# Performance work log

Hardware: AMD Instinct MI355X
Metric: run time of the kernel (lower is better)

The kernel has to match this reference:

```python
import jax, jax.numpy as jnp
from jax import lax
import numpy as np

PERCENTAGES = [0.004, 0.006, 0.008, 0.01, 0.012]
RADIUS = 1.0  # shape == 'square'
B, N = 4, 8192


def setup_inputs() -> dict:
    key = jax.random.key(0)
    adv_pcs = jax.random.uniform(key, (B, N, 3), dtype=jnp.float32)
    return {"adv_pcs": adv_pcs}


def _gather_points(pcs, idx):
    # pcs [B,N,3], idx [B,S] -> [B,S,3]
    idx3 = jnp.broadcast_to(idx[:, :, None], idx.shape + (3,))
    return jnp.take_along_axis(pcs, idx3, axis=1)


def farthest_point_sample(pcs, n_samples):
    # iterative FPS starting at index 0; returns indices [B, n_samples]
    Bb, Nn, _ = pcs.shape

    def step(carry, _):
        min_d2, last = carry  # [B,N], [B]
        p = _gather_points(pcs, last[:, None])  # [B,1,3]
        d2 = jnp.sum((pcs - p) ** 2, axis=-1)  # [B,N]
        min_d2 = jnp.minimum(min_d2, d2)
        nxt = jnp.argmax(min_d2, axis=-1).astype(jnp.int32)
        return (min_d2, nxt), last

    init = (jnp.full((Bb, Nn), 1e10, pcs.dtype), jnp.zeros((Bb,), jnp.int32))
    _, idx = lax.scan(step, init, None, length=n_samples)
    return jnp.transpose(idx)  # [B, n_samples]


def ball_query(seeds, pcs, r, K):
    # seeds [B,S,3], pcs [B,N,3] -> pts [B,S,K,3], idx [B,S,K] (-1 padded)
    d2 = jnp.sum((seeds[:, :, None, :] - pcs[:, None, :, :]) ** 2, axis=-1)  # [B,S,N]
    valid = d2 < r * r
    # stable sort: in-radius points first, preserving index order
    order = jnp.argsort(jnp.where(valid, 0, 1).astype(jnp.int32), axis=-1, stable=True)
    idx = order[..., :K]  # [B,S,K]
    cnt = jnp.sum(valid, axis=-1)  # [B,S]
    keep = jnp.arange(K)[None, None, :] < cnt[:, :, None]
    idx = jnp.where(keep, idx, -1)
    pts = jax.vmap(lambda p, i: p[i])(pcs, jnp.clip(idx, 0))  # [B,S,K,3]
    return pts, idx


def knn_second_sqdist(groups, lengths):
    # groups [G,K,3]; first `lengths[g]` rows of each group are valid candidates.
    # Returns squared distance to the 2nd nearest neighbor (incl. self at 0) [G,K].
    G, K, _ = groups.shape
    d2 = jnp.sum((groups[:, :, None, :] - groups[:, None, :, :]) ** 2, axis=-1)  # [G,K,K]
    col_ok = jnp.arange(K)[None, None, :] < lengths[:, None, None]
    d2 = jnp.where(col_ok, d2, jnp.inf)
    top2 = -lax.top_k(-d2, 2)[0]  # two smallest along candidates
    nn2 = top2[:, :, 1]  # second smallest (first is self, dist 0)
    return jnp.where(jnp.isfinite(nn2), nn2, 0.0)  # pad like pytorch3d (0 for missing)


def reference(adv_pcs):
    Bb, Nn, _ = adv_pcs.shape
    dt = adv_pcs.dtype
    seed_num = int(Nn * 0.05)
    fps_idx = farthest_point_sample(adv_pcs, seed_num)
    seeds = _gather_points(adv_pcs, fps_idx)  # [B,seed,3]
    loss = jnp.zeros((Bb,), dt)
    for p in PERCENTAGES:
        exp_num = Nn * p
        r = float(np.sqrt(p) * RADIUS)
        expect_dis = jnp.sqrt(jnp.asarray(np.pi * RADIUS ** 2 / exp_num * p, dt))
        K = int(2 * exp_num)
        pts, idx = ball_query(seeds, adv_pcs, r, K)
        pts = pts.reshape(Bb * seed_num, K, 3)
        idx = idx.reshape(Bb * seed_num, K)
        mask = idx != -1  # [G,K]
        gnum = jnp.sum(mask, axis=-1)  # [G], >= 1 (seed itself in-radius)
        nn2 = knn_second_sqdist(pts, gnum)  # [G,K] squared dists
        safe = jnp.where(nn2 > 0, nn2, 1.0)
        nn_dis = jnp.where(nn2 > 0, jnp.sqrt(safe), 0.0)
        clutter = jnp.square(nn_dis - expect_dis) / (expect_dis + 1e-12)
        # faithful to torch: sum over ALL elements, then elementwise divide by counts
        clutter_vec = jnp.sum(clutter * mask) / gnum.astype(dt)  # [G]
        imbalance = jnp.square(gnum.astype(dt) - exp_num) / exp_num  # [G]
        ul = (clutter_vec * imbalance).reshape(Bb, seed_num).mean(axis=-1)  # [B]
        loss = loss + ul
    return loss / len(PERCENTAGES)
```

## Files before the change

### kernel.cpp

```cpp
#include <hip/hip_runtime.h>
#include <math.h>

#define N_PTS 8192
#define B_SZ 4
#define SEED_NUM 409
#define FPS_THREADS 256
#define LTOT 653

typedef float f2 __attribute__((ext_vector_type(2)));
typedef float f4 __attribute__((ext_vector_type(4)));

__device__ __forceinline__ float sqdist(float ax, float ay, float az,
                                        float bx, float by, float bz) {
  float dx = __fsub_rn(ax, bx);
  float dy = __fsub_rn(ay, by);
  float dz = __fsub_rn(az, bz);
  return __fadd_rn(__fadd_rn(__fmul_rn(dx, dx), __fmul_rn(dy, dy)),
                   __fmul_rn(dz, dz));
}

#define FOR16(M) \
  M(0) M(1) M(2) M(3) M(4) M(5) M(6) M(7) \
  M(8) M(9) M(10) M(11) M(12) M(13) M(14) M(15)

template <int CTRL>
__device__ __forceinline__ unsigned long long dpp_u64_bc1(
    unsigned long long k) {
  const unsigned lo2 = (unsigned)__builtin_amdgcn_update_dpp(
      0, (int)(unsigned)k, CTRL, 0xf, 0xf, true);
  const unsigned hi2 = (unsigned)__builtin_amdgcn_update_dpp(
      0, (int)(unsigned)(k >> 32), CTRL, 0xf, 0xf, true);
  return ((unsigned long long)hi2 << 32) | lo2;
}
template <int CTRL, int ROW_MASK>
__device__ __forceinline__ unsigned long long dpp_u64_keep(
    unsigned long long k) {
  const unsigned lo2 = (unsigned)__builtin_amdgcn_update_dpp(
      (int)(unsigned)k, (int)(unsigned)k, CTRL, ROW_MASK, 0xf, false);
  const unsigned hi2 = (unsigned)__builtin_amdgcn_update_dpp(
      (int)(unsigned)(k >> 32), (int)(unsigned)(k >> 32), CTRL, ROW_MASK, 0xf,
      false);
  return ((unsigned long long)hi2 << 32) | lo2;
}

__global__ __launch_bounds__(FPS_THREADS, 1) void fps_kernel(
    const float* __restrict__ pcs, float* __restrict__ seeds,
    double* __restrict__ sums ) {
#pragma clang fp contract(off)
  const int b = blockIdx.x;
  const int tid = threadIdx.x;
  const int lane = tid & 63, wid = tid >> 6;
  const float* base = pcs + (size_t)b * N_PTS * 3;

  if (b == 0 && tid < 25) sums[tid] = 0.0;

  __shared__ f4 spts4[N_PTS];
  __shared__ float seedbuf[SEED_NUM * 3];
  __shared__ unsigned long long red[2][4];

#define FPS_DECL(j) f2 px##j, py##j, pz##j, md##j;
  FOR16(FPS_DECL)
#undef FPS_DECL

#define FPS_INIT(j)                                   \
  {                                                   \
    const int i0 = tid + (2 * (j)) * FPS_THREADS;     \
    const int i1 = i0 + FPS_THREADS;                  \
    px##j = (f2){base[i0 * 3 + 0], base[i1 * 3 + 0]}; \
    py##j = (f2){base[i0 * 3 + 1], base[i1 * 3 + 1]}; \
    pz##j = (f2){base[i0 * 3 + 2], base[i1 * 3 + 2]}; \
    md##j = (f2){1e10f, 1e10f};   \
    spts4[i0] = (f4){px##j.x, py##j.x, pz##j.x, 0.f}; \
    spts4[i1] = (f4){px##j.y, py##j.y, pz##j.y, 0.f}; \
  }
  FOR16(FPS_INIT)
#undef FPS_INIT

#define FPS_PIN(j) asm volatile("" : "+v"(px##j), "+v"(py##j), "+v"(pz##j));
  FOR16(FPS_PIN)
#undef FPS_PIN

  float cx = base[0], cy = base[1], cz = base[2];

  for (int s = 0; s < SEED_NUM; ++s) {
    if (tid == 0) {
      seedbuf[s * 3 + 0] = cx;
      seedbuf[s * 3 + 1] = cy;
      seedbuf[s * 3 + 2] = cz;
    }
    const f2 ccx = (f2){cx, cx}, ccy = (f2){cy, cy}, ccz = (f2){cz, cz};
    float bv = -1.0f;
    int bi = 0;
#define FPS_UPD(j)                                                      \
  {                                                                     \
    const f2 dx = px##j - ccx;                                          \
    const f2 dy = py##j - ccy;                                          \
    const f2 dz = pz##j - ccz;                                          \
    const f2 t0 = dx * dx;                                              \
    const f2 t1 = dy * dy;                                              \
    const f2 t2 = dz * dz;                                              \
    const f2 d2 = (t0 + t1) + t2;                                       \
    const f2 m = __builtin_elementwise_min(md##j, d2);                  \
    md##j = m;                                                          \
    if (m.x > bv) { bv = m.x; bi = tid + (2 * (j)) * FPS_THREADS; }     \
    if (m.y > bv) { bv = m.y; bi = tid + (2 * (j) + 1) * FPS_THREADS; } \
  }
    FOR16(FPS_UPD)
#undef FPS_UPD
    unsigned long long key =
        ((unsigned long long)__float_as_uint(bv) << 32) |
        (unsigned long long)(unsigned)(N_PTS - 1 - bi);
    unsigned long long o;
    o = dpp_u64_bc1<0x111>(key);         key = (o > key) ? o : key;
    o = dpp_u64_bc1<0x112>(key);         key = (o > key) ? o : key;
    o = dpp_u64_bc1<0x114>(key);         key = (o > key) ? o : key;
    o = dpp_u64_bc1<0x118>(key);         key = (o > key) ? o : key;
    o = dpp_u64_keep<0x142, 0xa>(key);   key = (o > key) ? o : key;
    o = dpp_u64_keep<0x143, 0xc>(key);   key = (o > key) ? o : key;
    if (lane == 63) red[s & 1][wid] = key;
    __syncthreads();
    unsigned long long kmax = red[s & 1][0];
#pragma unroll
    for (int w = 1; w < 4; ++w) {
      const unsigned long long t = red[s & 1][w];
      kmax = (t > kmax) ? t : kmax;
    }
    const int ci = N_PTS - 1 - (int)(unsigned)(kmax & 0xffffffffull);
    const f4 c = spts4[ci];
    cx = c.x;
    cy = c.y;
    cz = c.z;
  }

  __syncthreads();
  float* sg = seeds + (size_t)b * SEED_NUM * 3;
  for (int i = tid; i < SEED_NUM * 3; i += FPS_THREADS) sg[i] = seedbuf[i];
}

__global__ __launch_bounds__(256) void group_kernel(
    const float* __restrict__ pcs, const float* __restrict__ seeds,
    double* __restrict__ totS , double* __restrict__ accA ) {
  const int g = blockIdx.x;
  const int b = g / SEED_NUM;
  const int tid = threadIdx.x;
  const int lane = tid & 63, wid = tid >> 6;

  const int Kc[5] = {65, 98, 131, 163, 196};
  const int off[5] = {0, 65, 163, 294, 457};
  const double Pd[5] = {0.004, 0.006, 0.008, 0.01, 0.012};
  float r2c[5], expnf[5], expdc[5];
#pragma unroll
  for (int p = 0; p < 5; ++p) {
    const double pd = Pd[p];
    const double rd = sqrt(pd);
    r2c[p] = (float)(rd * rd);
    const double expn_d = 8192.0 * pd;
    expnf[p] = (float)expn_d;
    expdc[p] = sqrtf((float)(M_PI / expn_d * pd));
  }

  const float* base = pcs + (size_t)b * N_PTS * 3;
  const float* sp = seeds + (size_t)g * 3;
  const float sx = sp[0], sy = sp[1], sz = sp[2];

  __shared__ float lx[LTOT], ly[LTOT], lz[LTOT];
  __shared__ int cnt[5];
  __shared__ int wtot[4];
  __shared__ double wsum[4];

  if (tid < 5) cnt[tid] = 0;
  __syncthreads();

  const float r2max = r2c[4];
  for (int i = tid; i < N_PTS; i += 256) {
    const float x = base[i * 3 + 0];
    const float y = base[i * 3 + 1];
    const float z = base[i * 3 + 2];
    const float d2 = sqdist(x, y, z, sx, sy, sz);
    if (d2 < r2max) {
#pragma unroll
      for (int p = 0; p < 5; ++p) {
        if (d2 < r2c[p]) {
          const int pos = atomicAdd(&cnt[p], 1);
          if (pos < Kc[p]) {
            lx[off[p] + pos] = x;
            ly[off[p] + pos] = y;
            lz[off[p] + pos] = z;
          }
        }
      }
    }
  }
  __syncthreads();

#pragma unroll
  for (int p = 0; p < 5; ++p) {
    if (cnt[p] > Kc[p]) {
      int run = 0;
      for (int base_i = 0; base_i < N_PTS; base_i += 256) {
        const int i = base_i + tid;
        const float x = base[i * 3 + 0];
        const float y = base[i * 3 + 1];
        const float z = base[i * 3 + 2];
        const float d2 = sqdist(x, y, z, sx, sy, sz);
        const bool valid = d2 < r2c[p];
        const unsigned long long m = __ballot(valid);
        if (lane == 0) wtot[wid] = __popcll(m);
        __syncthreads();
        int pos = run + __popcll(m & ((1ull << lane) - 1ull));
        for (int w = 0; w < wid; ++w) pos += wtot[w];
        if (valid && pos < Kc[p]) {
          lx[off[p] + pos] = x; ly[off[p] + pos] = y; lz[off[p] + pos] = z;
        }
        run += wtot[0] + wtot[1] + wtot[2] + wtot[3];
        __syncthreads();
      }
    }
  }

#pragma unroll
  for (int p = 0; p < 5; ++p) {
    const int gn = min(cnt[p], Kc[p]);
    const float ed = expdc[p];
    const int lb = off[p];
    double localS = 0.0;
    for (int r0 = 0; r0 < gn; r0 += 64) {
      const int row = r0 + (tid >> 2);
      const int sub = tid & 3;
      float m1 = INFINITY, m2 = INFINITY;
      if (row < gn) {
        const float xi = lx[lb + row], yi = ly[lb + row], zi = lz[lb + row];
        for (int j = sub; j < gn; j += 4) {
          const float d2 = sqdist(xi, yi, zi, lx[lb + j], ly[lb + j], lz[lb + j]);
          if (d2 < m1) { m2 = m1; m1 = d2; }
          else if (d2 < m2) { m2 = d2; }
        }
      }
#pragma unroll
      for (int d = 1; d <= 2; d <<= 1) {
        const float om1 = __shfl_xor(m1, d);
        const float om2 = __shfl_xor(m2, d);
        const float lo = fminf(m1, om1);
        const float hi = fmaxf(m1, om1);
        m2 = fminf(fminf(m2, om2), hi);
        m1 = lo;
      }
      if (row < gn && sub == 0) {
        const float nn2 = (m2 > 1e37f) ? 0.0f : m2;
        const float nnd = (nn2 > 0.0f) ? sqrtf(nn2) : 0.0f;
        const float diff = __fsub_rn(nnd, ed);
        const float clut = __fdiv_rn(__fmul_rn(diff, diff),
                                     __fadd_rn(ed, 1e-12f));
        localS += (double)clut;
      }
    }
#pragma unroll
    for (int o = 32; o > 0; o >>= 1) localS += __shfl_down(localS, o);
    if (lane == 0) wsum[wid] = localS;
    __syncthreads();
    if (tid == 0) {
      const double S = wsum[0] + wsum[1] + wsum[2] + wsum[3];
      atomicAdd(&totS[p], S);
      const float gf = (float)gn;
      const float dd = __fsub_rn(gf, expnf[p]);
      const float imb = __fdiv_rn(__fmul_rn(dd, dd), expnf[p]);
      atomicAdd(&accA[p * 4 + b], (double)imb / (double)gf);
    }
    __syncthreads();
  }
}

__global__ void finalize_kernel(const double* __restrict__ totS,
                                const double* __restrict__ accA,
                                float* __restrict__ out) {
  const int b = threadIdx.x;
  if (b < B_SZ) {
    double acc = 0.0;
    for (int p = 0; p < 5; ++p)
      acc += totS[p] * (accA[p * 4 + b] / (double)SEED_NUM);
    out[b] = (float)(acc / 5.0);
  }
}

extern "C" void kernel_launch(void* const* d_in, const int* in_sizes, int n_in,
                              void* d_out, int out_size, void* d_ws,
                              size_t ws_size, hipStream_t stream) {
  (void)in_sizes; (void)n_in; (void)out_size; (void)ws_size;
  const float* pcs = (const float*)d_in[0];
  float* out = (float*)d_out;

  float* seeds = (float*)d_ws;
  double* sums = (double*)((char*)d_ws + 19632);

  fps_kernel<<<B_SZ, FPS_THREADS, 0, stream>>>(pcs, seeds, sums);
  group_kernel<<<B_SZ * SEED_NUM, 256, 0, stream>>>(pcs, seeds, sums, sums + 5);
  finalize_kernel<<<1, 64, 0, stream>>>(sums, sums + 5, out);
}
```

Baseline: 481.2 us.

## Fuse finalize into group kernel, pack points as float4, batch atomics

Removes the separate finalize launch: the last group block, detected through a global atomic counter, reads the accumulated sums and writes the output. Shared point storage moves from three SoA float arrays to a float4 array, so each neighbor is read with one vector LDS load. The per-percentage syncs and atomics are deferred to a single batched phase. The FPS reduction reads the four wave keys as two 128-bit loads. This adds a threadfence and counter atomic per block, and more shared memory for the float4 layout.

```diff
diff --git a/kernel.cpp b/kernel.cpp
--- a/kernel.cpp
+++ b/kernel.cpp
@@ -6,6 +6,7 @@
 #define SEED_NUM 409
 #define FPS_THREADS 256
 #define LTOT 653
+#define N_GROUPS (B_SZ * SEED_NUM)
 
 typedef float f2 __attribute__((ext_vector_type(2)));
 typedef float f4 __attribute__((ext_vector_type(4)));
@@ -52,11 +53,11 @@
   const int lane = tid & 63, wid = tid >> 6;
   const float* base = pcs + (size_t)b * N_PTS * 3;
 
-  if (b == 0 && tid < 25) sums[tid] = 0.0;
+  if (b == 0 && tid < 26) sums[tid] = 0.0;
 
   __shared__ f4 spts4[N_PTS];
   __shared__ float seedbuf[SEED_NUM * 3];
-  __shared__ unsigned long long red[2][4];
+  __shared__ __align__(16) unsigned long long red[2][4];
 
 #define FPS_DECL(j) f2 px##j, py##j, pz##j, md##j;
   FOR16(FPS_DECL)
@@ -119,12 +120,12 @@
     o = dpp_u64_keep<0x143, 0xc>(key);   key = (o > key) ? o : key;
     if (lane == 63) red[s & 1][wid] = key;
     __syncthreads();
-    unsigned long long kmax = red[s & 1][0];
-#pragma unroll
-    for (int w = 1; w < 4; ++w) {
-      const unsigned long long t = red[s & 1][w];
-      kmax = (t > kmax) ? t : kmax;
-    }
+    const ulonglong2* rp = (const ulonglong2*)(&red[s & 1][0]);
+    const ulonglong2 r01 = rp[0];
+    const ulonglong2 r23 = rp[1];
+    const unsigned long long ka = (r01.y > r01.x) ? r01.y : r01.x;
+    const unsigned long long kb = (r23.y > r23.x) ? r23.y : r23.x;
+    const unsigned long long kmax = (kb > ka) ? kb : ka;
     const int ci = N_PTS - 1 - (int)(unsigned)(kmax & 0xffffffffull);
     const f4 c = spts4[ci];
     cx = c.x;
@@ -139,7 +140,8 @@
 
 __global__ __launch_bounds__(256) void group_kernel(
     const float* __restrict__ pcs, const float* __restrict__ seeds,
-    double* __restrict__ totS , double* __restrict__ accA ) {
+    double* __restrict__ totS , double* __restrict__ accA ,
+    unsigned int* __restrict__ dcnt, float* __restrict__ out) {
   const int g = blockIdx.x;
   const int b = g / SEED_NUM;
   const int tid = threadIdx.x;
@@ -163,10 +165,11 @@
   const float* sp = seeds + (size_t)g * 3;
   const float sx = sp[0], sy = sp[1], sz = sp[2];
 
-  __shared__ float lx[LTOT], ly[LTOT], lz[LTOT];
+  __shared__ f4 lpt[LTOT];
   __shared__ int cnt[5];
   __shared__ int wtot[4];
-  __shared__ double wsum[4];
+  __shared__ double wsum[5][4];
+  __shared__ int islast;
 
   if (tid < 5) cnt[tid] = 0;
   __syncthreads();
@@ -183,9 +186,7 @@
         if (d2 < r2c[p]) {
           const int pos = atomicAdd(&cnt[p], 1);
           if (pos < Kc[p]) {
-            lx[off[p] + pos] = x;
-            ly[off[p] + pos] = y;
-            lz[off[p] + pos] = z;
+            lpt[off[p] + pos] = (f4){x, y, z, 0.f};
           }
         }
       }
@@ -210,7 +211,7 @@
         int pos = run + __popcll(m & ((1ull << lane) - 1ull));
         for (int w = 0; w < wid; ++w) pos += wtot[w];
         if (valid && pos < Kc[p]) {
-          lx[off[p] + pos] = x; ly[off[p] + pos] = y; lz[off[p] + pos] = z;
+          lpt[off[p] + pos] = (f4){x, y, z, 0.f};
         }
         run += wtot[0] + wtot[1] + wtot[2] + wtot[3];
         __syncthreads();
@@ -229,9 +230,10 @@
       const int sub = tid & 3;
       float m1 = INFINITY, m2 = INFINITY;
       if (row < gn) {
-        const float xi = lx[lb + row], yi = ly[lb + row], zi = lz[lb + row];
+        const f4 pi = lpt[lb + row];
         for (int j = sub; j < gn; j += 4) {
-          const float d2 = sqdist(xi, yi, zi, lx[lb + j], ly[lb + j], lz[lb + j]);
+          const f4 pj = lpt[lb + j];
+          const float d2 = sqdist(pi.x, pi.y, pi.z, pj.x, pj.y, pj.z);
           if (d2 < m1) { m2 = m1; m1 = d2; }
           else if (d2 < m2) { m2 = d2; }
         }
@@ -256,29 +258,43 @@
     }
 #pragma unroll
     for (int o = 32; o > 0; o >>= 1) localS += __shfl_down(localS, o);
-    if (lane == 0) wsum[wid] = localS;
+    if (lane == 0) wsum[p][wid] = localS;
+  }
+  __syncthreads();
+
+  if (tid < 5) {
+    const double S = wsum[tid][0] + wsum[tid][1] + wsum[tid][2] + wsum[tid][3];
+    atomicAdd(&totS[tid], S);
+  } else if (tid < 10) {
+    const int p = tid - 5;
+    const int gn = min(cnt[p], Kc[p]);
+    const float gf = (float)gn;
+    const float dd = __fsub_rn(gf, expnf[p]);
+    const float imb = __fdiv_rn(__fmul_rn(dd, dd), expnf[p]);
+    atomicAdd(&accA[p * 4 + b], (double)imb / (double)gf);
+  }
+
+  __syncthreads();
+  if (tid == 0) {
+    __threadfence();
+    const unsigned int old = atomicAdd(dcnt, 1u);
+    islast = (old == (unsigned int)(N_GROUPS - 1)) ? 1 : 0;
+  }
+  __syncthreads();
+  if (islast) {
+    __shared__ double fin[25];
+    if (tid < 25) {
+      const double* src = (tid < 5) ? &totS[tid] : &accA[tid - 5];
+      fin[tid] = atomicAdd((double*)src, 0.0);
+    }
     __syncthreads();
-    if (tid == 0) {
-      const double S = wsum[0] + wsum[1] + wsum[2] + wsum[3];
-      atomicAdd(&totS[p], S);
-      const float gf = (float)gn;
-      const float dd = __fsub_rn(gf, expnf[p]);
-      const float imb = __fdiv_rn(__fmul_rn(dd, dd), expnf[p]);
-      atomicAdd(&accA[p * 4 + b], (double)imb / (double)gf);
-    }
-    __syncthreads();
-  }
-}
-
-__global__ void finalize_kernel(const double* __restrict__ totS,
-                                const double* __restrict__ accA,
-                                float* __restrict__ out) {
-  const int b = threadIdx.x;
-  if (b < B_SZ) {
-    double acc = 0.0;
-    for (int p = 0; p < 5; ++p)
-      acc += totS[p] * (accA[p * 4 + b] / (double)SEED_NUM);
-    out[b] = (float)(acc / 5.0);
+    if (tid < B_SZ) {
+      double acc = 0.0;
+#pragma unroll
+      for (int p = 0; p < 5; ++p)
+        acc += fin[p] * (fin[5 + p * 4 + tid] / (double)SEED_NUM);
+      out[tid] = (float)(acc / 5.0);
+    }
   }
 }
 
@@ -293,6 +309,6 @@
   double* sums = (double*)((char*)d_ws + 19632);
 
   fps_kernel<<<B_SZ, FPS_THREADS, 0, stream>>>(pcs, seeds, sums);
-  group_kernel<<<B_SZ * SEED_NUM, 256, 0, stream>>>(pcs, seeds, sums, sums + 5);
-  finalize_kernel<<<1, 64, 0, stream>>>(sums, sums + 5, out);
-}
+  group_kernel<<<N_GROUPS, 256, 0, stream>>>(
+      pcs, seeds, sums, sums + 5, (unsigned int*)(sums + 25), out);
+}
```

Result: faster. 438.0 us (-9.0%).
